# Optimization experiments

Hardware: AMD Instinct MI355X
Metric: run time of the kernel (lower is better)

The kernel has to match this reference:

```python
import jax, jax.numpy as jnp
import numpy as np

EPS = 0.01
H = 256
W = 256
C = 3
RADIUS_PX = 1.5          # splat radius in pixels
K_PPP = 8                # points_per_pixel
RAD_POW = 2
TAU = 1                  # accumulation_tau
WIN = 5                  # 5x5 candidate pixel window per point (covers radius 1.5)


def make_xyzs():
    # matches torch buffer: rows are (x, y, 1, 1) over flattened (H, W)
    xs = jnp.arange(W, dtype=jnp.float32)
    ys = jnp.arange(H, dtype=jnp.float32)
    X, Y = jnp.meshgrid(xs, ys)  # (H, W), X varies along width
    ones = jnp.ones_like(X)
    return jnp.stack([X, Y, ones, ones], 0).reshape(1, 4, H * W)


def project_pts(pred_pts, Kmat, K_inv, RT_cam1, RTinv_cam2):
    # pred_pts: (bs, 1, N) depths
    xyzs = make_xyzs()
    proj = xyzs * pred_pts                       # (bs, 4, N)
    proj = proj.at[:, 3, :].set(1.0)
    cam1 = jnp.einsum('bij,bjn->bin', K_inv, proj)
    wrld = jnp.einsum('bij,bjn->bin', RT_cam1, cam1)
    newc = jnp.einsum('bij,bjn->bin', RTinv_cam2, wrld)
    xy = jnp.einsum('bij,bjn->bin', Kmat, newc)
    z = xy[:, 2:3]
    mask = jnp.abs(z) < EPS
    zs = jnp.where(mask, EPS, z)
    sx = xy[:, 0:1] / zs / float(W - 1) * 2.0 - 1.0
    sy = xy[:, 1:2] / zs / float(H - 1) * 2.0 - 1.0
    sampler = jnp.concatenate([sx, sy, z], 1)    # (bs, 3, N)
    sampler = jnp.where(mask, -10.0, sampler)
    return sampler


def splat_one(pts, alpha_pts, feats):
    # pts: (N,3) ndc x,y + depth z; alpha_pts: (N,); feats: (C,N)
    N = pts.shape[0]
    x = (pts[:, 0] + 1.0) * 0.5 * (W - 1)        # ndc -> pixel coords
    y = (pts[:, 1] + 1.0) * 0.5 * (H - 1)
    z = pts[:, 2]
    radius_ndc = RADIUS_PX / float(W) * 2.0
    px0 = jnp.floor(x).astype(jnp.int32)
    py0 = jnp.floor(y).astype(jnp.int32)
    offs = jnp.arange(WIN, dtype=jnp.int32) - WIN // 2
    oy, ox = jnp.meshgrid(offs, offs, indexing='ij')
    oy = oy.reshape(-1)
    ox = ox.reshape(-1)                           # (25,)
    py = py0[:, None] + oy[None, :]               # (N, 25)
    px = px0[:, None] + ox[None, :]
    d2_pix = (px.astype(jnp.float32) - x[:, None]) ** 2 + (py.astype(jnp.float32) - y[:, None]) ** 2
    inb = (px >= 0) & (px < W) & (py >= 0) & (py < H)
    valid = inb & (d2_pix <= RADIUS_PX ** 2) & (z[:, None] > 0.0)
    d2_ndc = d2_pix * (2.0 / float(W)) ** 2
    dist_norm = d2_ndc / (radius_ndc ** RAD_POW)
    a = (1.0 - jnp.sqrt(jnp.clip(dist_norm, 1e-3, 1.0))) ** TAU
    a = a * alpha_pts[:, None]
    a = jnp.where(valid, a, 0.0)
    pix = jnp.where(valid, py * W + px, H * W)    # invalid -> dump segment
    M = N * WIN * WIN
    pixf = pix.reshape(M)
    zf = jnp.broadcast_to(z[:, None], pix.shape).reshape(M)
    af = a.reshape(M)
    ptid = jnp.broadcast_to(jnp.arange(N, dtype=jnp.int32)[:, None], pix.shape).reshape(M)
    # depth-ordered z-buffer: sort by (pixel, z), keep first K per pixel
    order = jnp.lexsort((zf, pixf))
    pixs = pixf[order]
    as_ = af[order]
    ids = ptid[order]
    first = jnp.searchsorted(pixs, pixs, side='left')
    rank = jnp.arange(M) - first
    keep = (rank < K_PPP) & (pixs < H * W)
    slot = jnp.where(keep, pixs * K_PPP + rank, H * W * K_PPP)
    alpha_buf = jnp.zeros(H * W * K_PPP + 1, jnp.float32).at[slot].set(as_)[:-1].reshape(H * W, K_PPP)
    idx_buf = jnp.full(H * W * K_PPP + 1, -1, jnp.int32).at[slot].set(ids)[:-1].reshape(H * W, K_PPP)
    feat = feats[:, jnp.clip(idx_buf, 0)]         # (C, HW, K)
    feat = jnp.where(idx_buf[None] >= 0, feat, 0.0)
    # front-to-back alpha composite
    one_m = 1.0 - alpha_buf
    t_exc = jnp.concatenate([jnp.ones((H * W, 1), jnp.float32), jnp.cumprod(one_m, axis=1)[:, :-1]], axis=1)
    wgt = alpha_buf * t_exc                       # (HW, K)
    out = jnp.einsum('chk,hk->ch', feat, wgt)
    return out.reshape(C, H, W)


def setup_inputs() -> dict:
    key = jax.random.key(0)
    k1, k2, k3 = jax.random.split(key, 3)
    bs = 2
    src = jax.random.normal(k1, (bs, C, H, W), jnp.float32)
    pred_pts = jax.random.uniform(k2, (bs, 1, H, W), jnp.float32) * 7.0 + 1.0  # depths in [1, 8]
    alphas = jax.random.uniform(k3, (bs, 1, H, W), jnp.float32)
    f = float(W)
    Kn = np.array([[f, 0, W / 2.0, 0], [0, f, H / 2.0, 0], [0, 0, 1, 0], [0, 0, 0, 1]], np.float32)
    K_inv_n = np.linalg.inv(Kn).astype(np.float32)
    th = 0.05
    R = np.array([[np.cos(th), 0, np.sin(th), 0.1], [0, 1, 0, 0], [-np.sin(th), 0, np.cos(th), 0], [0, 0, 0, 1]], np.float32)
    I4 = np.eye(4, dtype=np.float32)
    tile = lambda m: jnp.asarray(np.broadcast_to(m, (bs, 4, 4)).copy())
    return {
        'alphas': alphas, 'src': src, 'pred_pts': pred_pts,
        'K': tile(Kn), 'K_inv': tile(K_inv_n),
        'RT_cam1': tile(I4), 'RTinv_cam1': tile(I4),
        'RT_cam2': tile(np.linalg.inv(R).astype(np.float32)), 'RTinv_cam2': tile(R),
    }


def reference(alphas, src, pred_pts, K, K_inv, RT_cam1, RTinv_cam1, RT_cam2, RTinv_cam2):
    bs, c = src.shape[0], src.shape[1]
    pred = pred_pts.reshape(bs, 1, -1)
    srcf = src.reshape(bs, c, -1)
    al = alphas.reshape(bs, -1)
    sampler = project_pts(pred, K, K_inv, RT_cam1, RTinv_cam2)
    pts = jnp.transpose(sampler, (0, 2, 1))       # (bs, N, 3)
    return jax.vmap(splat_one)(pts, al, srcf)     # (bs, C, H, W)
```

## Files before the change

### kernel.cpp

```cpp
#include <hip/hip_runtime.h>
#include <math.h>

#define HH 256
#define WW 256
#define NPIX (HH*WW)
#define GW (WW+4)
#define GH (HH+4)
#define NC (GW*GH)
#define CHUNK 256
#define NCHUNKS ((NC + CHUNK - 1) / CHUNK)
#define EPSF 0.01f
#define GATE 2.24997f

__device__ __forceinline__ float dot4(const float* M, int i, float a0, float a1, float a2, float a3) {
    float s = __fmul_rn(M[i*4+0], a0);
    s = __fadd_rn(s, __fmul_rn(M[i*4+1], a1));
    s = __fadd_rn(s, __fmul_rn(M[i*4+2], a2));
    s = __fadd_rn(s, __fmul_rn(M[i*4+3], a3));
    return s;
}

__global__ void zero_kernel(int4* __restrict__ p, int n4) {
    int i = blockIdx.x * blockDim.x + threadIdx.x;
    if (i < n4) p[i] = make_int4(0, 0, 0, 0);
}

__global__ void proj_kernel(const float* __restrict__ pred, const float* __restrict__ alphas,
                            const float* __restrict__ Kinv, const float* __restrict__ RT1,
                            const float* __restrict__ RTi2, const float* __restrict__ Km,
                            float4* __restrict__ pts, int* __restrict__ counts) {
    int b = blockIdx.y;
    int n = blockIdx.x * blockDim.x + threadIdx.x;
    __shared__ float Ms[4][16];
    int t = threadIdx.x;
    if (t < 64) {
        const float* srcs[4] = {Kinv, RT1, RTi2, Km};
        Ms[t >> 4][t & 15] = srcs[t >> 4][b*16 + (t & 15)];
    }
    __syncthreads();
    const float* KIs = Ms[0];
    const float* R1s = Ms[1];
    const float* R2s = Ms[2];
    const float* Ks  = Ms[3];

    float d = pred[b*NPIX + n];
    float X = (float)(n & (WW-1));
    float Y = (float)(n >> 8);
    float p0 = __fmul_rn(X, d);
    float p1 = __fmul_rn(Y, d);
    float p2 = d;
    float p3 = 1.0f;
    float c0 = dot4(KIs, 0, p0, p1, p2, p3);
    float c1 = dot4(KIs, 1, p0, p1, p2, p3);
    float c2 = dot4(KIs, 2, p0, p1, p2, p3);
    float c3 = dot4(KIs, 3, p0, p1, p2, p3);
    float w0 = dot4(R1s, 0, c0, c1, c2, c3);
    float w1 = dot4(R1s, 1, c0, c1, c2, c3);
    float w2 = dot4(R1s, 2, c0, c1, c2, c3);
    float w3 = dot4(R1s, 3, c0, c1, c2, c3);
    float q0 = dot4(R2s, 0, w0, w1, w2, w3);
    float q1 = dot4(R2s, 1, w0, w1, w2, w3);
    float q2 = dot4(R2s, 2, w0, w1, w2, w3);
    float q3 = dot4(R2s, 3, w0, w1, w2, w3);
    float xy0 = dot4(Ks, 0, q0, q1, q2, q3);
    float xy1 = dot4(Ks, 1, q0, q1, q2, q3);
    float z   = dot4(Ks, 2, q0, q1, q2, q3);

    bool mask = fabsf(z) < EPSF;
    float zs = mask ? EPSF : z;
    float tx = __fdiv_rn(xy0, zs);
    tx = __fdiv_rn(tx, 255.0f);
    tx = __fmul_rn(tx, 2.0f);
    float sx = __fsub_rn(tx, 1.0f);
    float ty = __fdiv_rn(xy1, zs);
    ty = __fdiv_rn(ty, 255.0f);
    ty = __fmul_rn(ty, 2.0f);
    float sy = __fsub_rn(ty, 1.0f);
    float sxm = mask ? -10.0f : sx;
    float sym = mask ? -10.0f : sy;
    float zo  = mask ? -10.0f : z;
    float x = __fmul_rn(__fmul_rn(__fadd_rn(sxm, 1.0f), 0.5f), 255.0f);
    float y = __fmul_rn(__fmul_rn(__fadd_rn(sym, 1.0f), 0.5f), 255.0f);

    float al = alphas[b*NPIX + n];
    pts[(size_t)b*NPIX + n] = make_float4(x, y, zo, al);

    if (zo > 0.0f) {
        float fx = floorf(x), fy = floorf(y);
        if (fx >= -2.0f && fx <= (float)(WW+1) && fy >= -2.0f && fy <= (float)(HH+1)) {
            int cx = (int)fx + 2, cy = (int)fy + 2;
            atomicAdd(&counts[(size_t)b*NC + cy*GW + cx], 1);
        }
    }
}

__global__ void scan_part(const int* __restrict__ counts, int* __restrict__ starts,
                          int* __restrict__ bsum) {
    int b = blockIdx.y;
    int chunk = blockIdx.x;
    int tid = threadIdx.x;
    int i = chunk*CHUNK + tid;
    int v = (i < NC) ? counts[(size_t)b*NC + i] : 0;
    __shared__ int sh[CHUNK];
    sh[tid] = v;
    __syncthreads();
    for (int off = 1; off < CHUNK; off <<= 1) {
        int t = (tid >= off) ? sh[tid - off] : 0;
        __syncthreads();
        sh[tid] += t;
        __syncthreads();
    }
    if (i < NC) starts[(size_t)b*(NC+1) + i] = sh[tid] - v;
    if (tid == CHUNK-1) bsum[b*NCHUNKS + chunk] = sh[tid];
}

__global__ void scan_add(int* __restrict__ starts, const int* __restrict__ bsum,
                         int* __restrict__ cursor) {
    int b = blockIdx.y;
    int chunk = blockIdx.x;
    int tid = threadIdx.x;
    __shared__ int sh[CHUNK];
    int v0 = (tid < chunk) ? bsum[b*NCHUNKS + tid] : 0;
    int i2 = tid + CHUNK;
    int v1 = (i2 < NCHUNKS && i2 < chunk) ? bsum[b*NCHUNKS + i2] : 0;
    sh[tid] = v0 + v1;
    __syncthreads();
    for (int off = CHUNK/2; off > 0; off >>= 1) {
        if (tid < off) sh[tid] += sh[tid + off];
        __syncthreads();
    }
    int offset = sh[0];
    int i = chunk*CHUNK + tid;
    if (i < NC) {
        int s = starts[(size_t)b*(NC+1) + i] + offset;
        starts[(size_t)b*(NC+1) + i] = s;
        cursor[(size_t)b*NC + i] = s;
    }
    if (chunk == NCHUNKS-1 && tid == 0)
        starts[(size_t)b*(NC+1) + NC] = offset + bsum[b*NCHUNKS + NCHUNKS-1];
}

__global__ void scatter_kernel(const float4* __restrict__ pts, int* __restrict__ cursor,
                               float4* __restrict__ bpts, int* __restrict__ bids,
                               const float* __restrict__ src, float4* __restrict__ rgb) {
    int b = blockIdx.y;
    int n = blockIdx.x * blockDim.x + threadIdx.x;
    float4 r = pts[(size_t)b*NPIX + n];
    float f0 = src[((size_t)b*3 + 0)*NPIX + n];
    float f1 = src[((size_t)b*3 + 1)*NPIX + n];
    float f2 = src[((size_t)b*3 + 2)*NPIX + n];
    rgb[(size_t)b*NPIX + n] = make_float4(f0, f1, f2, 0.f);
    if (r.z > 0.0f) {
        float fx = floorf(r.x), fy = floorf(r.y);
        if (fx >= -2.0f && fx <= (float)(WW+1) && fy >= -2.0f && fy <= (float)(HH+1)) {
            int cx = (int)fx + 2, cy = (int)fy + 2;
            int pos = atomicAdd(&cursor[(size_t)b*NC + cy*GW + cx], 1);
            bpts[(size_t)b*NPIX + pos] = r;
            bids[(size_t)b*NPIX + pos] = n;
        }
    }
}

__global__ void gather_kernel(const float4* __restrict__ bpts, const int* __restrict__ starts,
                              const int* __restrict__ bids, const float4* __restrict__ rgb,
                              float* __restrict__ out) {
    int b = blockIdx.y;
    int p = blockIdx.x * blockDim.x + threadIdx.x;
    int px = p & (WW-1);
    int py = p >> 8;
    const int* st = starts + (size_t)b*(NC+1);
    const int* ids = bids + (size_t)b*NPIX;
    const float4* B = bpts + (size_t)b*NPIX;

    float zz[8]; int ii[8]; float aa[8];
#pragma unroll
    for (int k = 0; k < 8; ++k) { zz[k] = INFINITY; ii[k] = 0x7fffffff; aa[k] = 0.f; }

    float fpx = (float)px, fpy = (float)py;
    for (int cy = py; cy <= py + 4; ++cy) {
        int base = cy*GW + px;
        int s = st[base];
        int e = st[base + 5];
        for (int j = s; j < e; ++j) {
            float4 r = B[j];
            float dx = __fsub_rn(fpx, r.x);
            float dy = __fsub_rn(fpy, r.y);
            float d2 = __fadd_rn(__fmul_rn(dx, dx), __fmul_rn(dy, dy));
            if (!(d2 <= GATE)) continue;
            int n = ids[j];
            float dn = __fdiv_rn(d2, 2.25f);
            dn = fminf(fmaxf(dn, 0.001f), 1.0f);
            float ta = __fmul_rn(__fsub_rn(1.0f, sqrtf(dn)), r.w);
            float tz = r.z; int tn = n;
#pragma unroll
            for (int k = 0; k < 8; ++k) {
                bool lt = (tz < zz[k]) || (tz == zz[k] && tn < ii[k]);
                float oz = zz[k]; int oi = ii[k]; float oa = aa[k];
                zz[k] = lt ? tz : oz;  ii[k] = lt ? tn : oi;  aa[k] = lt ? ta : oa;
                tz = lt ? oz : tz;     tn = lt ? oi : tn;     ta = lt ? oa : ta;
            }
        }
    }

    const float4* F = rgb + (size_t)b*NPIX;
    float T = 1.0f, c0 = 0.f, c1 = 0.f, c2 = 0.f;
#pragma unroll
    for (int k = 0; k < 8; ++k) {
        int n = ii[k];
        if (n != 0x7fffffff) {
            float wgt = __fmul_rn(aa[k], T);
            float4 f = F[n];
            c0 = __fadd_rn(c0, __fmul_rn(wgt, f.x));
            c1 = __fadd_rn(c1, __fmul_rn(wgt, f.y));
            c2 = __fadd_rn(c2, __fmul_rn(wgt, f.z));
            T = __fmul_rn(T, __fsub_rn(1.0f, aa[k]));
        }
    }
    out[((size_t)b*3 + 0)*NPIX + p] = c0;
    out[((size_t)b*3 + 1)*NPIX + p] = c1;
    out[((size_t)b*3 + 2)*NPIX + p] = c2;
}

extern "C" void kernel_launch(void* const* d_in, const int* in_sizes, int n_in,
                              void* d_out, int out_size, void* d_ws, size_t ws_size,
                              hipStream_t stream) {
    const float* alphas = (const float*)d_in[0];
    const float* src    = (const float*)d_in[1];
    const float* pred   = (const float*)d_in[2];
    const float* Kmat   = (const float*)d_in[3];
    const float* Kinv   = (const float*)d_in[4];
    const float* RT1    = (const float*)d_in[5];
    const float* RTinv2 = (const float*)d_in[8];
    float* out = (float*)d_out;

    int bs = in_sizes[0] / NPIX;

    char* w = (char*)d_ws;
    size_t need = 0;
    float4* pts   = (float4*)(w);                 need += (size_t)bs*NPIX*sizeof(float4);
    float4* bpts  = (float4*)(w + need);          need += (size_t)bs*NPIX*sizeof(float4);
    float4* rgb   = (float4*)(w + need);          need += (size_t)bs*NPIX*sizeof(float4);
    int*    cnts  = (int*)(w + need);             need += (size_t)bs*NC*sizeof(int);
    int*    strts = (int*)(w + need);             need += (size_t)bs*(NC+1)*sizeof(int);
    int*    curs  = (int*)(w + need);             need += (size_t)bs*NC*sizeof(int);
    int*    bids  = (int*)(w + need);             need += (size_t)bs*NPIX*sizeof(int);
    int*    bsum  = (int*)(w + need);             need += (size_t)bs*NCHUNKS*sizeof(int);
    if (ws_size < need) return;

    int n4 = bs*NC/4;
    zero_kernel<<<(n4 + 255)/256, 256, 0, stream>>>((int4*)cnts, n4);
    proj_kernel<<<dim3(NPIX/256, bs), 256, 0, stream>>>(pred, alphas, Kinv, RT1, RTinv2, Kmat, pts, cnts);
    scan_part<<<dim3(NCHUNKS, bs), CHUNK, 0, stream>>>(cnts, strts, bsum);
    scan_add<<<dim3(NCHUNKS, bs), CHUNK, 0, stream>>>(strts, bsum, curs);
    scatter_kernel<<<dim3(NPIX/256, bs), 256, 0, stream>>>(pts, curs, bpts, bids, src, rgb);
    gather_kernel<<<dim3(NPIX/256, bs), 256, 0, stream>>>(bpts, strts, bids, rgb, out);
}
```

Before: 63.00 us.

## Split gather candidate scan across two threads per pixel with LDS top-8 merge

Each output pixel is now handled by two threads. Each thread scans half of every bin row's candidate range and keeps its own sorted top-8 list. The second thread writes its list to shared memory, and the first merges the two sorted lists before compositing. The start/end offsets are also loaded up front. This doubles the thread count to hide memory latency and shorten the serial insertion chain per thread. The cost is a block barrier, shared-memory traffic, and half the threads sitting idle during compositing.

```diff
diff --git a/kernel.cpp b/kernel.cpp
--- a/kernel.cpp
+++ b/kernel.cpp
@@ -165,23 +165,36 @@
                               const int* __restrict__ bids, const float4* __restrict__ rgb,
                               float* __restrict__ out) {
     int b = blockIdx.y;
-    int p = blockIdx.x * blockDim.x + threadIdx.x;
+    int lp = threadIdx.x & 127;
+    int w  = threadIdx.x >> 7;
+    int p  = blockIdx.x * 128 + lp;
     int px = p & (WW-1);
     int py = p >> 8;
     const int* st = starts + (size_t)b*(NC+1);
     const int* ids = bids + (size_t)b*NPIX;
     const float4* B = bpts + (size_t)b*NPIX;
 
+    int s0[5], e0[5];
+#pragma unroll
+    for (int r5 = 0; r5 < 5; ++r5) {
+        int base = (py + r5)*GW + px;
+        s0[r5] = st[base];
+        e0[r5] = st[base + 5];
+    }
+
     float zz[8]; int ii[8]; float aa[8];
 #pragma unroll
     for (int k = 0; k < 8; ++k) { zz[k] = INFINITY; ii[k] = 0x7fffffff; aa[k] = 0.f; }
 
     float fpx = (float)px, fpy = (float)py;
-    for (int cy = py; cy <= py + 4; ++cy) {
-        int base = cy*GW + px;
-        int s = st[base];
-        int e = st[base + 5];
-        for (int j = s; j < e; ++j) {
+#pragma unroll
+    for (int r5 = 0; r5 < 5; ++r5) {
+        int s = s0[r5], e = e0[r5];
+        int cnt = e - s;
+        int half = (cnt + 1) >> 1;
+        int js = w ? (s + half) : s;
+        int je = w ? e : (s + half);
+        for (int j = js; j < je; ++j) {
             float4 r = B[j];
             float dx = __fsub_rn(fpx, r.x);
             float dy = __fsub_rn(fpy, r.y);
@@ -202,23 +215,46 @@
         }
     }
 
-    const float4* F = rgb + (size_t)b*NPIX;
-    float T = 1.0f, c0 = 0.f, c1 = 0.f, c2 = 0.f;
-#pragma unroll
-    for (int k = 0; k < 8; ++k) {
-        int n = ii[k];
-        if (n != 0x7fffffff) {
-            float wgt = __fmul_rn(aa[k], T);
-            float4 f = F[n];
-            c0 = __fadd_rn(c0, __fmul_rn(wgt, f.x));
-            c1 = __fadd_rn(c1, __fmul_rn(wgt, f.y));
-            c2 = __fadd_rn(c2, __fmul_rn(wgt, f.z));
-            T = __fmul_rn(T, __fsub_rn(1.0f, aa[k]));
-        }
-    }
-    out[((size_t)b*3 + 0)*NPIX + p] = c0;
-    out[((size_t)b*3 + 1)*NPIX + p] = c1;
-    out[((size_t)b*3 + 2)*NPIX + p] = c2;
+    __shared__ float mz[128][8];
+    __shared__ int   mi[128][8];
+    __shared__ float ma[128][8];
+    if (w == 1) {
+#pragma unroll
+        for (int k = 0; k < 8; ++k) { mz[lp][k] = zz[k]; mi[lp][k] = ii[k]; ma[lp][k] = aa[k]; }
+    }
+    __syncthreads();
+    if (w == 0) {
+        float fz[8]; int fi[8]; float fa[8];
+        int ia = 0, ib = 0;
+#pragma unroll
+        for (int k = 0; k < 8; ++k) {
+            float za = zz[ia]; int na = ii[ia];
+            float zb = mz[lp][ib]; int nb = mi[lp][ib];
+            bool ta = (za < zb) || (za == zb && na < nb);
+            fz[k] = ta ? za : zb;
+            fi[k] = ta ? na : nb;
+            fa[k] = ta ? aa[ia] : ma[lp][ib];
+            ia += ta ? 1 : 0;
+            ib += ta ? 0 : 1;
+        }
+        const float4* F = rgb + (size_t)b*NPIX;
+        float T = 1.0f, c0 = 0.f, c1 = 0.f, c2 = 0.f;
+#pragma unroll
+        for (int k = 0; k < 8; ++k) {
+            int n = fi[k];
+            if (n != 0x7fffffff) {
+                float wgt = __fmul_rn(fa[k], T);
+                float4 f = F[n];
+                c0 = __fadd_rn(c0, __fmul_rn(wgt, f.x));
+                c1 = __fadd_rn(c1, __fmul_rn(wgt, f.y));
+                c2 = __fadd_rn(c2, __fmul_rn(wgt, f.z));
+                T = __fmul_rn(T, __fsub_rn(1.0f, fa[k]));
+            }
+        }
+        out[((size_t)b*3 + 0)*NPIX + p] = c0;
+        out[((size_t)b*3 + 1)*NPIX + p] = c1;
+        out[((size_t)b*3 + 2)*NPIX + p] = c2;
+    }
 }
 
 extern "C" void kernel_launch(void* const* d_in, const int* in_sizes, int n_in,
@@ -253,5 +289,5 @@
     scan_part<<<dim3(NCHUNKS, bs), CHUNK, 0, stream>>>(cnts, strts, bsum);
     scan_add<<<dim3(NCHUNKS, bs), CHUNK, 0, stream>>>(strts, bsum, curs);
     scatter_kernel<<<dim3(NPIX/256, bs), 256, 0, stream>>>(pts, curs, bpts, bids, src, rgb);
-    gather_kernel<<<dim3(NPIX/256, bs), 256, 0, stream>>>(bpts, strts, bids, rgb, out);
-}
+    gather_kernel<<<dim3(NPIX/128, bs), 256, 0, stream>>>(bpts, strts, bids, rgb, out);
+}
```

After: 56.71 us. 1.11x faster.

## Tile gather kernel 16x16 and stage binned points in shared memory

Applied to the files above, without the earlier changes.

The gather kernel now processes 16x16 pixel tiles instead of linear rows of 256 pixels. Each block first loads the bin offsets for its 20 padded rows and the binned point data (split into SoA arrays) into LDS, so that neighbouring pixels reuse the same points without repeated global loads. Rows holding more than 64 points fall back to reading from global memory. This adds two block-wide barriers and about 27 KB of LDS per block, which may lower occupancy. The serial per-row staging loop also adds latency before any compute starts.

```diff
diff --git a/kernel.cpp b/kernel.cpp
--- a/kernel.cpp
+++ b/kernel.cpp
@@ -11,6 +11,9 @@
 #define NCHUNKS ((NC + CHUNK - 1) / CHUNK)
 #define EPSF 0.01f
 #define GATE 2.24997f
+#define TILE 16
+#define ROWS (TILE + 4)
+#define CAP 64
 
 __device__ __forceinline__ float dot4(const float* M, int i, float a0, float a1, float a2, float a3) {
     float s = __fmul_rn(M[i*4+0], a0);
@@ -164,40 +167,98 @@
 __global__ void gather_kernel(const float4* __restrict__ bpts, const int* __restrict__ starts,
                               const int* __restrict__ bids, const float4* __restrict__ rgb,
                               float* __restrict__ out) {
-    int b = blockIdx.y;
-    int p = blockIdx.x * blockDim.x + threadIdx.x;
-    int px = p & (WW-1);
-    int py = p >> 8;
+    int b   = blockIdx.z;
+    int tx0 = blockIdx.x * TILE;
+    int ty0 = blockIdx.y * TILE;
+    int tid = threadIdx.x;
     const int* st = starts + (size_t)b*(NC+1);
     const int* ids = bids + (size_t)b*NPIX;
     const float4* B = bpts + (size_t)b*NPIX;
 
+    __shared__ int   soffs[ROWS][TILE+5];
+    __shared__ int   rowbig[ROWS];
+    __shared__ float lpx[ROWS][CAP];
+    __shared__ float lpy[ROWS][CAP];
+    __shared__ float lpz[ROWS][CAP];
+    __shared__ float lpa[ROWS][CAP];
+    __shared__ int   lid[ROWS][CAP];
+
+    for (int t = tid; t < ROWS*(TILE+5); t += 256) {
+        int r = t / (TILE+5), i = t - r*(TILE+5);
+        soffs[r][i] = st[(ty0 + r)*GW + tx0 + i];
+    }
+    __syncthreads();
+    for (int r = 0; r < ROWS; ++r) {
+        int s = soffs[r][0];
+        int c = soffs[r][TILE+4] - s;
+        if (c <= CAP) {
+            if (tid == 0) rowbig[r] = 0;
+            for (int t = tid; t < c; t += 256) {
+                float4 v = B[s + t];
+                lpx[r][t] = v.x; lpy[r][t] = v.y; lpz[r][t] = v.z; lpa[r][t] = v.w;
+                lid[r][t] = ids[s + t];
+            }
+        } else {
+            if (tid == 0) rowbig[r] = 1;
+        }
+    }
+    __syncthreads();
+
+    int lx = tid & (TILE-1);
+    int ly = tid >> 4;
+    int px = tx0 + lx;
+    int py = ty0 + ly;
+
     float zz[8]; int ii[8]; float aa[8];
 #pragma unroll
     for (int k = 0; k < 8; ++k) { zz[k] = INFINITY; ii[k] = 0x7fffffff; aa[k] = 0.f; }
 
     float fpx = (float)px, fpy = (float)py;
-    for (int cy = py; cy <= py + 4; ++cy) {
-        int base = cy*GW + px;
-        int s = st[base];
-        int e = st[base + 5];
-        for (int j = s; j < e; ++j) {
-            float4 r = B[j];
-            float dx = __fsub_rn(fpx, r.x);
-            float dy = __fsub_rn(fpy, r.y);
-            float d2 = __fadd_rn(__fmul_rn(dx, dx), __fmul_rn(dy, dy));
-            if (!(d2 <= GATE)) continue;
-            int n = ids[j];
-            float dn = __fdiv_rn(d2, 2.25f);
-            dn = fminf(fmaxf(dn, 0.001f), 1.0f);
-            float ta = __fmul_rn(__fsub_rn(1.0f, sqrtf(dn)), r.w);
-            float tz = r.z; int tn = n;
-#pragma unroll
-            for (int k = 0; k < 8; ++k) {
-                bool lt = (tz < zz[k]) || (tz == zz[k] && tn < ii[k]);
-                float oz = zz[k]; int oi = ii[k]; float oa = aa[k];
-                zz[k] = lt ? tz : oz;  ii[k] = lt ? tn : oi;  aa[k] = lt ? ta : oa;
-                tz = lt ? oz : tz;     tn = lt ? oi : tn;     ta = lt ? oa : ta;
+#pragma unroll
+    for (int dy = 0; dy < 5; ++dy) {
+        int r = ly + dy;
+        int jS = soffs[r][lx];
+        int jE = soffs[r][lx + 5];
+        if (!rowbig[r]) {
+            int base0 = soffs[r][0];
+            for (int j = jS; j < jE; ++j) {
+                int t = j - base0;
+                float rx = lpx[r][t], ry = lpy[r][t];
+                float dx = __fsub_rn(fpx, rx);
+                float dy2 = __fsub_rn(fpy, ry);
+                float d2 = __fadd_rn(__fmul_rn(dx, dx), __fmul_rn(dy2, dy2));
+                if (!(d2 <= GATE)) continue;
+                float dn = __fdiv_rn(d2, 2.25f);
+                dn = fminf(fmaxf(dn, 0.001f), 1.0f);
+                float ta = __fmul_rn(__fsub_rn(1.0f, sqrtf(dn)), lpa[r][t]);
+                float tz = lpz[r][t]; int tn = lid[r][t];
+#pragma unroll
+                for (int k = 0; k < 8; ++k) {
+                    bool lt = (tz < zz[k]) || (tz == zz[k] && tn < ii[k]);
+                    float oz = zz[k]; int oi = ii[k]; float oa = aa[k];
+                    zz[k] = lt ? tz : oz;  ii[k] = lt ? tn : oi;  aa[k] = lt ? ta : oa;
+                    tz = lt ? oz : tz;     tn = lt ? oi : tn;     ta = lt ? oa : ta;
+                }
+            }
+        } else {
+            for (int j = jS; j < jE; ++j) {
+                float4 v = B[j];
+                float dx = __fsub_rn(fpx, v.x);
+                float dy2 = __fsub_rn(fpy, v.y);
+                float d2 = __fadd_rn(__fmul_rn(dx, dx), __fmul_rn(dy2, dy2));
+                if (!(d2 <= GATE)) continue;
+                int n = ids[j];
+                float dn = __fdiv_rn(d2, 2.25f);
+                dn = fminf(fmaxf(dn, 0.001f), 1.0f);
+                float ta = __fmul_rn(__fsub_rn(1.0f, sqrtf(dn)), v.w);
+                float tz = v.z; int tn = n;
+#pragma unroll
+                for (int k = 0; k < 8; ++k) {
+                    bool lt = (tz < zz[k]) || (tz == zz[k] && tn < ii[k]);
+                    float oz = zz[k]; int oi = ii[k]; float oa = aa[k];
+                    zz[k] = lt ? tz : oz;  ii[k] = lt ? tn : oi;  aa[k] = lt ? ta : oa;
+                    tz = lt ? oz : tz;     tn = lt ? oi : tn;     ta = lt ? oa : ta;
+                }
             }
         }
     }
@@ -216,6 +277,7 @@
             T = __fmul_rn(T, __fsub_rn(1.0f, aa[k]));
         }
     }
+    int p = py*WW + px;
     out[((size_t)b*3 + 0)*NPIX + p] = c0;
     out[((size_t)b*3 + 1)*NPIX + p] = c1;
     out[((size_t)b*3 + 2)*NPIX + p] = c2;
@@ -253,5 +315,5 @@
     scan_part<<<dim3(NCHUNKS, bs), CHUNK, 0, stream>>>(cnts, strts, bsum);
     scan_add<<<dim3(NCHUNKS, bs), CHUNK, 0, stream>>>(strts, bsum, curs);
     scatter_kernel<<<dim3(NPIX/256, bs), 256, 0, stream>>>(pts, curs, bpts, bids, src, rgb);
-    gather_kernel<<<dim3(NPIX/256, bs), 256, 0, stream>>>(bpts, strts, bids, rgb, out);
-}
+    gather_kernel<<<dim3(WW/TILE, HH/TILE, bs), 256, 0, stream>>>(bpts, strts, bids, rgb, out);
+}
```

After: 62.04 us. About the same (-1.5%).

## Split per-pixel candidate scan across four lanes with shared-memory top-8 merge

Applied to the files above, without the earlier changes.

The gather kernel now gives each pixel four threads. Each thread strides through the binned candidate points and keeps its own sorted top-8 list. The four partial lists go to shared memory and one lane per pixel does a 4-way merge to produce the final 8 nearest points, then composites. This adds parallelism to the divergent, serial candidate loop, which is likely the bottleneck. In exchange it adds shared-memory traffic, a block-wide sync, 4x the threads and idle lanes during the merge.

```diff
diff --git a/kernel.cpp b/kernel.cpp
--- a/kernel.cpp
+++ b/kernel.cpp
@@ -164,10 +164,13 @@
 __global__ void gather_kernel(const float4* __restrict__ bpts, const int* __restrict__ starts,
                               const int* __restrict__ bids, const float4* __restrict__ rgb,
                               float* __restrict__ out) {
-    int b = blockIdx.y;
-    int p = blockIdx.x * blockDim.x + threadIdx.x;
-    int px = p & (WW-1);
-    int py = p >> 8;
+    int b   = blockIdx.y;
+    int tid = threadIdx.x;
+    int lp  = tid >> 2;
+    int q   = tid & 3;
+    int p   = blockIdx.x * 64 + lp;
+    int px  = p & (WW-1);
+    int py  = p >> 8;
     const int* st = starts + (size_t)b*(NC+1);
     const int* ids = bids + (size_t)b*NPIX;
     const float4* B = bpts + (size_t)b*NPIX;
@@ -177,11 +180,12 @@
     for (int k = 0; k < 8; ++k) { zz[k] = INFINITY; ii[k] = 0x7fffffff; aa[k] = 0.f; }
 
     float fpx = (float)px, fpy = (float)py;
-    for (int cy = py; cy <= py + 4; ++cy) {
-        int base = cy*GW + px;
+#pragma unroll
+    for (int r5 = 0; r5 < 5; ++r5) {
+        int base = (py + r5)*GW + px;
         int s = st[base];
         int e = st[base + 5];
-        for (int j = s; j < e; ++j) {
+        for (int j = s + q; j < e; j += 4) {
             float4 r = B[j];
             float dx = __fsub_rn(fpx, r.x);
             float dy = __fsub_rn(fpy, r.y);
@@ -202,23 +206,45 @@
         }
     }
 
-    const float4* F = rgb + (size_t)b*NPIX;
-    float T = 1.0f, c0 = 0.f, c1 = 0.f, c2 = 0.f;
-#pragma unroll
-    for (int k = 0; k < 8; ++k) {
-        int n = ii[k];
-        if (n != 0x7fffffff) {
-            float wgt = __fmul_rn(aa[k], T);
-            float4 f = F[n];
-            c0 = __fadd_rn(c0, __fmul_rn(wgt, f.x));
-            c1 = __fadd_rn(c1, __fmul_rn(wgt, f.y));
-            c2 = __fadd_rn(c2, __fmul_rn(wgt, f.z));
-            T = __fmul_rn(T, __fsub_rn(1.0f, aa[k]));
-        }
-    }
-    out[((size_t)b*3 + 0)*NPIX + p] = c0;
-    out[((size_t)b*3 + 1)*NPIX + p] = c1;
-    out[((size_t)b*3 + 2)*NPIX + p] = c2;
+    __shared__ float mz[64][4][8];
+    __shared__ int   mi[64][4][8];
+    __shared__ float ma[64][4][8];
+#pragma unroll
+    for (int k = 0; k < 8; ++k) { mz[lp][q][k] = zz[k]; mi[lp][q][k] = ii[k]; ma[lp][q][k] = aa[k]; }
+    __syncthreads();
+
+    if (q == 0) {
+        int p0 = 0, p1 = 0, p2 = 0, p3 = 0;
+        const float4* F = rgb + (size_t)b*NPIX;
+        float T = 1.0f, c0 = 0.f, c1 = 0.f, c2 = 0.f;
+#pragma unroll
+        for (int k = 0; k < 8; ++k) {
+            float z0 = mz[lp][0][p0]; int n0 = mi[lp][0][p0];
+            float z1 = mz[lp][1][p1]; int n1 = mi[lp][1][p1];
+            float z2 = mz[lp][2][p2]; int n2 = mi[lp][2][p2];
+            float z3 = mz[lp][3][p3]; int n3 = mi[lp][3][p3];
+            bool t01 = (z1 < z0) || (z1 == z0 && n1 < n0);
+            float za = t01 ? z1 : z0; int na = t01 ? n1 : n0; int sa = t01 ? 1 : 0;
+            bool t23 = (z3 < z2) || (z3 == z2 && n3 < n2);
+            float zb = t23 ? z3 : z2; int nb = t23 ? n3 : n2; int sb = t23 ? 3 : 2;
+            bool tab = (zb < za) || (zb == za && nb < na);
+            int sel = tab ? sb : sa;
+            int nm  = tab ? nb : na;
+            float am = ma[lp][sel][tab ? (t23 ? p3 : p2) : (t01 ? p1 : p0)];
+            p0 += (sel == 0); p1 += (sel == 1); p2 += (sel == 2); p3 += (sel == 3);
+            if (nm != 0x7fffffff) {
+                float wgt = __fmul_rn(am, T);
+                float4 f = F[nm];
+                c0 = __fadd_rn(c0, __fmul_rn(wgt, f.x));
+                c1 = __fadd_rn(c1, __fmul_rn(wgt, f.y));
+                c2 = __fadd_rn(c2, __fmul_rn(wgt, f.z));
+                T = __fmul_rn(T, __fsub_rn(1.0f, am));
+            }
+        }
+        out[((size_t)b*3 + 0)*NPIX + p] = c0;
+        out[((size_t)b*3 + 1)*NPIX + p] = c1;
+        out[((size_t)b*3 + 2)*NPIX + p] = c2;
+    }
 }
 
 extern "C" void kernel_launch(void* const* d_in, const int* in_sizes, int n_in,
@@ -253,5 +279,5 @@
     scan_part<<<dim3(NCHUNKS, bs), CHUNK, 0, stream>>>(cnts, strts, bsum);
     scan_add<<<dim3(NCHUNKS, bs), CHUNK, 0, stream>>>(strts, bsum, curs);
     scatter_kernel<<<dim3(NPIX/256, bs), 256, 0, stream>>>(pts, curs, bpts, bids, src, rgb);
-    gather_kernel<<<dim3(NPIX/256, bs), 256, 0, stream>>>(bpts, strts, bids, rgb, out);
-}
+    gather_kernel<<<dim3(NPIX/64, bs), 256, 0, stream>>>(bpts, strts, bids, rgb, out);
+}
```

Result: faster. 57.21 us (-9.2%).
